# Kernel tuning notes

Measured on AMD Instinct MI355X. Metric: run time of the kernel, lower is better.

## Reference

```python
import jax, jax.numpy as jnp
import numpy as np

L, F, H, T, C, N = 6, 256, 8, 256, 4, 16
HD = F // H
E = 4 * F
D = T * F * C
NS = 2


def setup_inputs() -> dict:
    key = jax.random.key(0)
    ks = iter(jax.random.split(key, 64))
    rn = lambda shape, s=0.02: (jax.random.normal(next(ks), shape, jnp.float32) * s)
    inp = {
        'x': jax.random.normal(next(ks), (N, F, T, C), jnp.float32),
        'Wq': rn((L, HD, HD)), 'Wk': rn((L, HD, HD)), 'Wv': rn((L, HD, HD)),
        'Wo': rn((L, F, F)), 'bo': jnp.zeros((L, F), jnp.float32),
        'ln1_g': jnp.ones((L, F), jnp.float32), 'ln1_b': jnp.zeros((L, F), jnp.float32),
        'ln2_g': jnp.ones((L, F), jnp.float32), 'ln2_b': jnp.zeros((L, F), jnp.float32),
        'ffW1': rn((L, E, F)), 'ffb1': jnp.zeros((L, E), jnp.float32),
        'ffW2': rn((L, F, E)), 'ffb2': jnp.zeros((L, F), jnp.float32),
        'eW1': rn((256, D), 0.005), 'eb1': jnp.zeros((256,), jnp.float32),
        'eg': jnp.ones((256,), jnp.float32), 'ebt': jnp.zeros((256,), jnp.float32),
        'eW2': rn((256, 256)), 'eb2': jnp.zeros((256,), jnp.float32),
        'eW3': rn((256, 256)), 'eb3': jnp.zeros((256,), jnp.float32),
        'eW4': rn((NS, 256)),
        'aW1': rn((256, D), 0.005), 'ab1': jnp.zeros((256,), jnp.float32),
        'ag': jnp.ones((256,), jnp.float32), 'abt': jnp.zeros((256,), jnp.float32),
        'aW2': rn((256, 256)), 'ab2': jnp.zeros((256,), jnp.float32),
        'aW3': rn((256, 256)), 'ab3': jnp.zeros((256,), jnp.float32),
        'aW4': rn((2, 256)),
    }
    return inp


def _layernorm(z, g, b):
    m = z.mean(-1, keepdims=True)
    v = z.var(-1, keepdims=True)
    return (z - m) / jnp.sqrt(v + 1e-5) * g + b


def _forward(x, Wq, Wk, Wv, Wo, bo, ln1_g, ln1_b, ln2_g, ln2_b,
             ffW1, ffb1, ffW2, ffb2,
             eW1, eb1, eg, ebt, eW2, eb2, eW3, eb3, eW4,
             aW1, ab1, ag, abt, aW2, ab2, aW3, ab3, aW4):
    n, f, t, c = x.shape
    # fold cues into batch: (C*N, T, F)
    h = jnp.transpose(x, (3, 0, 2, 1)).reshape(c * n, t, f)
    pos = jnp.linspace(0.0, 1.0, t, dtype=jnp.float32)[None, :, None]  # linspace over time, same per freq
    h = h + pos
    scale = 1.0 / jnp.sqrt(jnp.float32(f))
    for l in range(Wq.shape[0]):
        zr = h.reshape(h.shape[0], t, H, HD)
        q = zr @ Wq[l].T
        k = zr @ Wk[l].T
        v = zr @ Wv[l].T
        att = jax.nn.softmax(jnp.einsum('nqhd,nkhd->nhqk', q, k) * scale, axis=-1)
        o = jnp.einsum('nhqk,nkhd->nqhd', att, v).reshape(h.shape[0], t, f)
        o = o @ Wo[l].T + bo[l]
        x1 = _layernorm(o + h, ln1_g[l], ln1_b[l])
        ff = jax.nn.relu(x1 @ ffW1[l].T + ffb1[l]) @ ffW2[l].T + ffb2[l]
        h = _layernorm(ff + x1, ln2_g[l], ln2_b[l])
    enc = h.reshape(c, n, t, f).transpose(1, 2, 3, 0)  # (N, T, F, C)
    flat = enc.reshape(n, -1)

    def head(W1, b1, g, bt, W2, b2, W3, b3, W4):
        z = flat @ W1.T + b1
        z = z / jnp.sqrt(1.0 + 1e-5) * g + bt  # eval BatchNorm1d, running stats (0, 1)
        z = jax.nn.relu(z)
        z = jax.nn.relu(z @ W2.T + b2)
        z = jax.nn.relu(z @ W3.T + b3)
        return z @ W4.T

    pi = np.float32(np.pi)
    elev = jnp.clip(head(eW1, eb1, eg, ebt, eW2, eb2, eW3, eb3, eW4), -pi / 4, pi / 2)
    azim = jnp.clip(head(aW1, ab1, ag, abt, aW2, ab2, aW3, ab3, aW4), 0.0, 2 * pi)
    cols = []
    for i in range(elev.shape[1]):
        cols.append(elev[:, i])
        cols.append(azim[:, i])
    return jnp.stack(cols, axis=-1)  # (N, 2*Nsound)


def reference(x, Wq, Wk, Wv, Wo, bo, ln1_g, ln1_b, ln2_g, ln2_b,
              ffW1, ffb1, ffW2, ffb2,
              eW1, eb1, eg, ebt, eW2, eb2, eW3, eb3, eW4,
              aW1, ab1, ag, abt, aW2, ab2, aW3, ab3, aW4):
    return _forward(x, Wq, Wk, Wv, Wo, bo, ln1_g, ln1_b, ln2_g, ln2_b,
                    ffW1, ffb1, ffW2, ffb2,
                    eW1, eb1, eg, ebt, eW2, eb2, eW3, eb3, eW4,
                    aW1, ab1, ag, abt, aW2, ab2, aW3, ab3, aW4)
```

## Files before the change

### kernel.cpp

```cpp
#include <hip/hip_runtime.h>
#include <math.h>

#define T_ 256
#define F_ 256
#define B_ 64
#define H_ 8
#define HD_ 32
#define E_ 1024
#define D_ 262144
#define N_ 16
#define M_ 16384

typedef __attribute__((ext_vector_type(8))) short bf16x8;
typedef __attribute__((ext_vector_type(4))) float f32x4;

__global__ __launch_bounds__(256) void build_h(const float* __restrict__ x,
                                               float* __restrict__ h) {
    int idx = blockIdx.x * 256 + threadIdx.x;
    int f = idx & 255;
    int t = (idx >> 8) & 255;
    int b = idx >> 16;
    int c = b >> 4;
    int n = b & 15;
    h[idx] = x[((n * 256 + f) * 256 + t) * 4 + c] + (float)t * (1.0f / 255.0f);
}

__global__ __launch_bounds__(256) void attn_kernel(const float* __restrict__ h,
                                                   const float* __restrict__ Wq,
                                                   const float* __restrict__ Wk,
                                                   const float* __restrict__ Wv,
                                                   float* __restrict__ o) {
    __shared__ float ks[256][32];
    __shared__ float vs[256][32];
    const int b = blockIdx.x >> 3;
    const int hh = blockIdx.x & 7;
    const int t = threadIdx.x;

    const float* zp = h + (b * 256 + t) * 256 + hh * 32;
    float z[32];
#pragma unroll
    for (int e4 = 0; e4 < 8; ++e4) {
        float4 tv = *(const float4*)(zp + e4 * 4);
        z[e4 * 4 + 0] = tv.x; z[e4 * 4 + 1] = tv.y;
        z[e4 * 4 + 2] = tv.z; z[e4 * 4 + 3] = tv.w;
    }

    float q[32];
#pragma unroll
    for (int dg = 0; dg < 8; ++dg) {
        float4 k4, v4;
#pragma unroll
        for (int di = 0; di < 4; ++di) {
            const int d = dg * 4 + di;
            const float* wq = Wq + d * 32;
            const float* wk = Wk + d * 32;
            const float* wv = Wv + d * 32;
            float qd = 0.f, kd = 0.f, vd = 0.f;
#pragma unroll
            for (int e = 0; e < 32; ++e) {
                qd += z[e] * wq[e];
                kd += z[e] * wk[e];
                vd += z[e] * wv[e];
            }
            q[d] = qd * 0.0625f;
            (&k4.x)[di] = kd;
            (&v4.x)[di] = vd;
        }
        *(float4*)&ks[t][dg * 4] = k4;
        *(float4*)&vs[t][dg * 4] = v4;
    }
    __syncthreads();

    float m = -1e30f, lsum = 0.f;
    float oacc[32];
#pragma unroll
    for (int e = 0; e < 32; ++e) oacc[e] = 0.f;

    for (int j = 0; j < 256; ++j) {
        const float4* kp = (const float4*)&ks[j][0];
        float s = 0.f;
#pragma unroll
        for (int e4 = 0; e4 < 8; ++e4) {
            float4 kv = kp[e4];
            s += q[e4 * 4 + 0] * kv.x + q[e4 * 4 + 1] * kv.y +
                 q[e4 * 4 + 2] * kv.z + q[e4 * 4 + 3] * kv.w;
        }
        float mn = fmaxf(m, s);
        float alpha = __expf(m - mn);
        float p = __expf(s - mn);
        lsum = lsum * alpha + p;
        const float4* vp = (const float4*)&vs[j][0];
#pragma unroll
        for (int e4 = 0; e4 < 8; ++e4) {
            float4 vv = vp[e4];
            oacc[e4 * 4 + 0] = oacc[e4 * 4 + 0] * alpha + p * vv.x;
            oacc[e4 * 4 + 1] = oacc[e4 * 4 + 1] * alpha + p * vv.y;
            oacc[e4 * 4 + 2] = oacc[e4 * 4 + 2] * alpha + p * vv.z;
            oacc[e4 * 4 + 3] = oacc[e4 * 4 + 3] * alpha + p * vv.w;
        }
        m = mn;
    }
    const float inv = 1.0f / lsum;
    float* op = o + (b * 256 + t) * 256 + hh * 32;
#pragma unroll
    for (int e4 = 0; e4 < 8; ++e4) {
        float4 ov;
        ov.x = oacc[e4 * 4 + 0] * inv; ov.y = oacc[e4 * 4 + 1] * inv;
        ov.z = oacc[e4 * 4 + 2] * inv; ov.w = oacc[e4 * 4 + 3] * inv;
        *(float4*)(op + e4 * 4) = ov;
    }
}

#define LDST 40

struct GemmLds {
    short Ahi[128][LDST];
    short Alo[128][LDST];
    short Whi[128][LDST];
    short Wlo[128][LDST];
};

__device__ inline void split2(float a0, float a1, unsigned& hi, unsigned& lo) {
    unsigned u0 = __float_as_uint(a0), u1 = __float_as_uint(a1);
    hi = __builtin_amdgcn_perm(u1, u0, 0x07060302);
    float r0 = a0 - __uint_as_float(u0 & 0xffff0000u);
    float r1 = a1 - __uint_as_float(u1 & 0xffff0000u);
    lo = __builtin_amdgcn_perm(__float_as_uint(r1), __float_as_uint(r0), 0x07060302);
}

__global__ __launch_bounds__(256, 2) void gemm_mfma(const float* __restrict__ A,
                                                    const float* __restrict__ W,
                                                    const float* __restrict__ bias,
                                                    float* __restrict__ C,
                                                    int M, int Nn, int K, int doRelu) {
    __shared__ GemmLds lds;
    const int tid = threadIdx.x;
    const int row0 = blockIdx.y * 128, col0 = blockIdx.x * 128;
    const int wave = tid >> 6, lane = tid & 63;
    const int wr = wave >> 1, wc = wave & 1;
    const int lrow = tid >> 3;
    const int lcol = (tid & 7) * 4;

    f32x4 acc[4][4];
#pragma unroll
    for (int i = 0; i < 4; ++i)
#pragma unroll
        for (int j = 0; j < 4; ++j) acc[i][j] = (f32x4){0.f, 0.f, 0.f, 0.f};

    float4 abuf[4], wbuf[4];
#pragma unroll
    for (int jj = 0; jj < 4; ++jj) {
        abuf[jj] = *(const float4*)&A[(size_t)(row0 + jj * 32 + lrow) * K + lcol];
        wbuf[jj] = *(const float4*)&W[(size_t)(col0 + jj * 32 + lrow) * K + lcol];
    }

    for (int k0 = 0; k0 < K; k0 += 32) {
#pragma unroll
        for (int jj = 0; jj < 4; ++jj) {
            const int row = jj * 32 + lrow;
            unsigned h01, l01, h23, l23;
            split2(abuf[jj].x, abuf[jj].y, h01, l01);
            split2(abuf[jj].z, abuf[jj].w, h23, l23);
            *(uint2*)&lds.Ahi[row][lcol] = make_uint2(h01, h23);
            *(uint2*)&lds.Alo[row][lcol] = make_uint2(l01, l23);
            split2(wbuf[jj].x, wbuf[jj].y, h01, l01);
            split2(wbuf[jj].z, wbuf[jj].w, h23, l23);
            *(uint2*)&lds.Whi[row][lcol] = make_uint2(h01, h23);
            *(uint2*)&lds.Wlo[row][lcol] = make_uint2(l01, l23);
        }
        __syncthreads();

        if (k0 + 32 < K) {
#pragma unroll
            for (int jj = 0; jj < 4; ++jj) {
                abuf[jj] = *(const float4*)&A[(size_t)(row0 + jj * 32 + lrow) * K + k0 + 32 + lcol];
                wbuf[jj] = *(const float4*)&W[(size_t)(col0 + jj * 32 + lrow) * K + k0 + 32 + lcol];
            }
        }

        const int fr = lane & 15, koff = (lane >> 4) * 8;
        bf16x8 ahi[4], alo[4], whi[4], wlo[4];
#pragma unroll
        for (int i = 0; i < 4; ++i) {
            ahi[i] = *(const bf16x8*)&lds.Ahi[wr * 64 + i * 16 + fr][koff];
            alo[i] = *(const bf16x8*)&lds.Alo[wr * 64 + i * 16 + fr][koff];
        }
#pragma unroll
        for (int j = 0; j < 4; ++j) {
            whi[j] = *(const bf16x8*)&lds.Whi[wc * 64 + j * 16 + fr][koff];
            wlo[j] = *(const bf16x8*)&lds.Wlo[wc * 64 + j * 16 + fr][koff];
        }
#pragma unroll
        for (int i = 0; i < 4; ++i)
#pragma unroll
            for (int j = 0; j < 4; ++j) {
                acc[i][j] = __builtin_amdgcn_mfma_f32_16x16x32_bf16(alo[i], whi[j], acc[i][j], 0, 0, 0);
                acc[i][j] = __builtin_amdgcn_mfma_f32_16x16x32_bf16(ahi[i], wlo[j], acc[i][j], 0, 0, 0);
                acc[i][j] = __builtin_amdgcn_mfma_f32_16x16x32_bf16(ahi[i], whi[j], acc[i][j], 0, 0, 0);
            }
        __syncthreads();
    }

    const int fr = lane & 15, rg = (lane >> 4) * 4;
#pragma unroll
    for (int j = 0; j < 4; ++j) {
        const int col = col0 + wc * 64 + j * 16 + fr;
        const float bv = bias[col];
#pragma unroll
        for (int i = 0; i < 4; ++i) {
#pragma unroll
            for (int r = 0; r < 4; ++r) {
                const int row = row0 + wr * 64 + i * 16 + rg + r;
                float v = acc[i][j][r] + bv;
                if (doRelu) v = fmaxf(v, 0.f);
                C[(size_t)row * Nn + col] = v;
            }
        }
    }
}

__global__ __launch_bounds__(256) void ln_residual(const float* __restrict__ A,
                                                   const float* __restrict__ R,
                                                   const float* __restrict__ g,
                                                   const float* __restrict__ b,
                                                   float* __restrict__ O) {
    const int row = blockIdx.x;
    const int tid = threadIdx.x;
    float v = A[row * 256 + tid] + R[row * 256 + tid];
    float s = v, sq = v * v;
#pragma unroll
    for (int off = 32; off > 0; off >>= 1) {
        s += __shfl_down(s, off, 64);
        sq += __shfl_down(sq, off, 64);
    }
    __shared__ float ss[4], ssq[4];
    const int wave = tid >> 6, lane = tid & 63;
    if (lane == 0) { ss[wave] = s; ssq[wave] = sq; }
    __syncthreads();
    float S = ss[0] + ss[1] + ss[2] + ss[3];
    float SQ = ssq[0] + ssq[1] + ssq[2] + ssq[3];
    float mean = S * (1.0f / 256.0f);
    float var = SQ * (1.0f / 256.0f) - mean * mean;
    float inv = rsqrtf(var + 1e-5f);
    O[row * 256 + tid] = (v - mean) * inv * g[tid] + b[tid];
}

__global__ __launch_bounds__(256) void head_gemm(const float* __restrict__ h,
                                                 const float* __restrict__ eW1,
                                                 const float* __restrict__ aW1,
                                                 float* __restrict__ zraw) {
    const int bx = blockIdx.x;
    const int jt = bx >> 4;
    const int chunk = bx & 15;
    const int jj0 = jt * 4;
    const int head = jj0 >> 8;
    const int jl0 = jj0 & 255;
    const float* W = (head ? aW1 : eW1) + (size_t)jl0 * D_;
    const int tid = threadIdx.x;

    float acc[4][16];
#pragma unroll
    for (int jb = 0; jb < 4; ++jb)
#pragma unroll
        for (int n = 0; n < 16; ++n) acc[jb][n] = 0.f;

    for (int s = 0; s < 16; ++s) {
        const int d4 = chunk * 16384 + s * 1024 + tid * 4;
        const int tf = d4 >> 2;
        float4 wv[4];
#pragma unroll
        for (int jb = 0; jb < 4; ++jb)
            wv[jb] = *(const float4*)(W + (size_t)jb * D_ + d4);
#pragma unroll
        for (int c = 0; c < 4; ++c) {
            const float* hp = h + c * 1048576 + tf;
            float fl[16];
#pragma unroll
            for (int n = 0; n < 16; ++n) fl[n] = hp[n * 65536];
#pragma unroll
            for (int jb = 0; jb < 4; ++jb) {
                const float w = (&wv[jb].x)[c];
#pragma unroll
                for (int n = 0; n < 16; ++n) acc[jb][n] += w * fl[n];
            }
        }
    }

    const int lane = tid & 63;
#pragma unroll
    for (int jb = 0; jb < 4; ++jb) {
#pragma unroll
        for (int n = 0; n < 16; ++n) {
            float v = acc[jb][n];
            v += __shfl_down(v, 32, 64);
            v += __shfl_down(v, 16, 64);
            v += __shfl_down(v, 8, 64);
            v += __shfl_down(v, 4, 64);
            v += __shfl_down(v, 2, 64);
            v += __shfl_down(v, 1, 64);
            if (lane == 0)
                atomicAdd(&zraw[head * 4096 + n * 256 + jl0 + jb], v);
        }
    }
}

__global__ __launch_bounds__(256) void zero_kernel(float* __restrict__ p) {
    p[blockIdx.x * 256 + threadIdx.x] = 0.f;
}

__global__ __launch_bounds__(256) void mlp_head(const float* __restrict__ zr,
                                                const float* __restrict__ b1,
                                                const float* __restrict__ g,
                                                const float* __restrict__ bt,
                                                const float* __restrict__ W2,
                                                const float* __restrict__ b2,
                                                const float* __restrict__ W3,
                                                const float* __restrict__ b3,
                                                const float* __restrict__ W4,
                                                float* __restrict__ out,
                                                float lo, float hi, int coff) {
    __shared__ float za[256], zb[256];
    const int n = blockIdx.x, j = threadIdx.x;
    float z = zr[n * 256 + j] + b1[j];
    z = z * 0.99999500003749969f * g[j] + bt[j];
    za[j] = fmaxf(z, 0.f);
    __syncthreads();
    float a = b2[j];
    for (int e = 0; e < 256; ++e) a += za[e] * W2[j * 256 + e];
    zb[j] = fmaxf(a, 0.f);
    __syncthreads();
    a = b3[j];
    for (int e = 0; e < 256; ++e) a += zb[e] * W3[j * 256 + e];
    za[j] = fmaxf(a, 0.f);
    __syncthreads();
    if (j < 2) {
        float v = 0.f;
        for (int e = 0; e < 256; ++e) v += za[e] * W4[j * 256 + e];
        v = fminf(fmaxf(v, lo), hi);
        out[n * 4 + 2 * j + coff] = v;
    }
}

extern "C" void kernel_launch(void* const* d_in, const int* in_sizes, int n_in,
                              void* d_out, int out_size, void* d_ws, size_t ws_size,
                              hipStream_t stream) {
    const float* x     = (const float*)d_in[0];
    const float* Wq    = (const float*)d_in[1];
    const float* Wk    = (const float*)d_in[2];
    const float* Wv    = (const float*)d_in[3];
    const float* Wo    = (const float*)d_in[4];
    const float* bo    = (const float*)d_in[5];
    const float* ln1g  = (const float*)d_in[6];
    const float* ln1b  = (const float*)d_in[7];
    const float* ln2g  = (const float*)d_in[8];
    const float* ln2b  = (const float*)d_in[9];
    const float* ffW1  = (const float*)d_in[10];
    const float* ffb1  = (const float*)d_in[11];
    const float* ffW2  = (const float*)d_in[12];
    const float* ffb2  = (const float*)d_in[13];
    const float* eW1   = (const float*)d_in[14];
    const float* eb1   = (const float*)d_in[15];
    const float* eg    = (const float*)d_in[16];
    const float* ebt   = (const float*)d_in[17];
    const float* eW2   = (const float*)d_in[18];
    const float* eb2   = (const float*)d_in[19];
    const float* eW3   = (const float*)d_in[20];
    const float* eb3   = (const float*)d_in[21];
    const float* eW4   = (const float*)d_in[22];
    const float* aW1   = (const float*)d_in[23];
    const float* ab1   = (const float*)d_in[24];
    const float* ag    = (const float*)d_in[25];
    const float* abt   = (const float*)d_in[26];
    const float* aW2   = (const float*)d_in[27];
    const float* ab2   = (const float*)d_in[28];
    const float* aW3   = (const float*)d_in[29];
    const float* ab3   = (const float*)d_in[30];
    const float* aW4   = (const float*)d_in[31];
    float* out = (float*)d_out;

    float* ws   = (float*)d_ws;
    float* h    = ws;
    float* ao   = ws + 4194304;
    float* tmp  = ws + 8388608;
    float* x1   = ws + 12582912;
    float* ff1  = ws + 16777216;
    float* zraw = ws + 33554432;

    build_h<<<16384, 256, 0, stream>>>(x, h);

    for (int l = 0; l < 6; ++l) {
        attn_kernel<<<512, 256, 0, stream>>>(h, Wq + l * 1024, Wk + l * 1024,
                                             Wv + l * 1024, ao);
        gemm_mfma<<<dim3(2, 128), 256, 0, stream>>>(ao, Wo + l * 65536, bo + l * 256,
                                                    tmp, M_, 256, 256, 0);
        ln_residual<<<16384, 256, 0, stream>>>(tmp, h, ln1g + l * 256, ln1b + l * 256, x1);
        gemm_mfma<<<dim3(8, 128), 256, 0, stream>>>(x1, ffW1 + l * 262144, ffb1 + l * 1024,
                                                    ff1, M_, 1024, 256, 1);
        gemm_mfma<<<dim3(2, 128), 256, 0, stream>>>(ff1, ffW2 + l * 262144, ffb2 + l * 256,
                                                    tmp, M_, 256, 1024, 0);
        ln_residual<<<16384, 256, 0, stream>>>(tmp, x1, ln2g + l * 256, ln2b + l * 256, h);
    }

    zero_kernel<<<32, 256, 0, stream>>>(zraw);
    head_gemm<<<2048, 256, 0, stream>>>(h, eW1, aW1, zraw);

    const float pi = 3.14159265358979323846f;
    mlp_head<<<16, 256, 0, stream>>>(zraw, eb1, eg, ebt, eW2, eb2, eW3, eb3, eW4,
                                     out, -pi / 4.f, pi / 2.f, 0);
    mlp_head<<<16, 256, 0, stream>>>(zraw + 4096, ab1, ag, abt, aW2, ab2, aW3, ab3, aW4,
                                     out, 0.f, 2.f * pi, 1);
}
```

Measured before the change: 2.555 ms.

## Restructure head GEMM to stage activations in shared memory and split by K-chunk

The big head GEMM (512x262144 weights against 16 batch rows) is reorganised. Each block now stages a 256-element slice of the encoder output for all 64 (cue, batch) columns in LDS and reuses it across all 256 output rows of one head. Previously every block re-read strided activations from global memory. Each thread handles 4 output rows for one cue, and results are reduced with xor shuffles across 4 lanes before atomics into zraw. The change also shrinks the grid from 2048 to 512 blocks, with more work per block and more atomics per block.

```diff
diff --git a/kernel.cpp b/kernel.cpp
--- a/kernel.cpp
+++ b/kernel.cpp
@@ -249,58 +249,72 @@
                                                  const float* __restrict__ eW1,
                                                  const float* __restrict__ aW1,
                                                  float* __restrict__ zraw) {
-    const int bx = blockIdx.x;
-    const int jt = bx >> 4;
-    const int chunk = bx & 15;
-    const int jj0 = jt * 4;
-    const int head = jj0 >> 8;
-    const int jl0 = jj0 & 255;
-    const float* W = (head ? aW1 : eW1) + (size_t)jl0 * D_;
+    __shared__ float hs[256][64];
     const int tid = threadIdx.x;
-
-    float acc[4][16];
-#pragma unroll
-    for (int jb = 0; jb < 4; ++jb)
-#pragma unroll
-        for (int n = 0; n < 16; ++n) acc[jb][n] = 0.f;
-
-    for (int s = 0; s < 16; ++s) {
-        const int d4 = chunk * 16384 + s * 1024 + tid * 4;
-        const int tf = d4 >> 2;
-        float4 wv[4];
-#pragma unroll
-        for (int jb = 0; jb < 4; ++jb)
-            wv[jb] = *(const float4*)(W + (size_t)jb * D_ + d4);
-#pragma unroll
-        for (int c = 0; c < 4; ++c) {
-            const float* hp = h + c * 1048576 + tf;
-            float fl[16];
-#pragma unroll
-            for (int n = 0; n < 16; ++n) fl[n] = hp[n * 65536];
-#pragma unroll
-            for (int jb = 0; jb < 4; ++jb) {
-                const float w = (&wv[jb].x)[c];
-#pragma unroll
-                for (int n = 0; n < 16; ++n) acc[jb][n] += w * fl[n];
+    const int jt = blockIdx.x >> 8;
+    const int kc = blockIdx.x & 255;
+    const int tf0 = kc * 256;
+
+    {
+        const int w = tid >> 6;
+        const int cn = tid & 63;
+        const int c = cn >> 4, n = cn & 15;
+        const float* hp = h + c * 1048576 + n * 65536 + tf0 + w * 64;
+#pragma unroll
+        for (int k4 = 0; k4 < 16; ++k4) {
+            float4 hv = *(const float4*)(hp + k4 * 4);
+            hs[w * 64 + k4 * 4 + 0][cn] = hv.x;
+            hs[w * 64 + k4 * 4 + 1][cn] = hv.y;
+            hs[w * 64 + k4 * 4 + 2][cn] = hv.z;
+            hs[w * 64 + k4 * 4 + 3][cn] = hv.w;
+        }
+    }
+    __syncthreads();
+
+    const int jg = tid >> 2;
+    const int c = tid & 3;
+    const float* Wp = (jt ? aW1 : eW1) + (size_t)(jg * 4) * D_ + kc * 1024 + c;
+
+    f32x4 acc[4][4];
+#pragma unroll
+    for (int jj = 0; jj < 4; ++jj)
+#pragma unroll
+        for (int n4 = 0; n4 < 4; ++n4) acc[jj][n4] = (f32x4){0.f, 0.f, 0.f, 0.f};
+
+#pragma unroll 4
+    for (int i = 0; i < 256; ++i) {
+        const float w0 = Wp[i * 4];
+        const float w1 = Wp[i * 4 + D_];
+        const float w2 = Wp[i * 4 + 2 * D_];
+        const float w3 = Wp[i * 4 + 3 * D_];
+        const f32x4* hv = (const f32x4*)&hs[i][c * 16];
+        const f32x4 h0 = hv[0], h1 = hv[1], h2 = hv[2], h3 = hv[3];
+        acc[0][0] += w0 * h0; acc[0][1] += w0 * h1; acc[0][2] += w0 * h2; acc[0][3] += w0 * h3;
+        acc[1][0] += w1 * h0; acc[1][1] += w1 * h1; acc[1][2] += w1 * h2; acc[1][3] += w1 * h3;
+        acc[2][0] += w2 * h0; acc[2][1] += w2 * h1; acc[2][2] += w2 * h2; acc[2][3] += w2 * h3;
+        acc[3][0] += w3 * h0; acc[3][1] += w3 * h1; acc[3][2] += w3 * h2; acc[3][3] += w3 * h3;
+    }
+
+#pragma unroll
+    for (int jj = 0; jj < 4; ++jj)
+#pragma unroll
+        for (int n4 = 0; n4 < 4; ++n4)
+#pragma unroll
+            for (int q = 0; q < 4; ++q) {
+                float v = acc[jj][n4][q];
+                v += __shfl_xor(v, 1, 64);
+                v += __shfl_xor(v, 2, 64);
+                acc[jj][n4][q] = v;
             }
-        }
-    }
-
-    const int lane = tid & 63;
-#pragma unroll
-    for (int jb = 0; jb < 4; ++jb) {
-#pragma unroll
-        for (int n = 0; n < 16; ++n) {
-            float v = acc[jb][n];
-            v += __shfl_down(v, 32, 64);
-            v += __shfl_down(v, 16, 64);
-            v += __shfl_down(v, 8, 64);
-            v += __shfl_down(v, 4, 64);
-            v += __shfl_down(v, 2, 64);
-            v += __shfl_down(v, 1, 64);
-            if (lane == 0)
-                atomicAdd(&zraw[head * 4096 + n * 256 + jl0 + jb], v);
-        }
+    if (c == 0) {
+        float* zp = zraw + jt * 4096 + jg * 4;
+#pragma unroll
+        for (int jj = 0; jj < 4; ++jj)
+#pragma unroll
+            for (int n4 = 0; n4 < 4; ++n4)
+#pragma unroll
+                for (int q = 0; q < 4; ++q)
+                    atomicAdd(&zp[(n4 * 4 + q) * 256 + jj], acc[jj][n4][q]);
     }
 }
 
@@ -402,7 +416,7 @@
     }
 
     zero_kernel<<<32, 256, 0, stream>>>(zraw);
-    head_gemm<<<2048, 256, 0, stream>>>(h, eW1, aW1, zraw);
+    head_gemm<<<512, 256, 0, stream>>>(h, eW1, aW1, zraw);
 
     const float pi = 3.14159265358979323846f;
     mlp_head<<<16, 256, 0, stream>>>(zraw, eb1, eg, ebt, eW2, eb2, eW3, eb3, eW4,
```

Result: no change. 2.580 ms (+1.0%).

## Run head GEMM on bf16 MFMA with hi/lo split-precision emulation

Applied to the files above, without the earlier changes.

Replaces the scalar FP32 FMA head GEMM (16 samples × 512 outputs × 262144 reduction) with an MFMA kernel. The activations are pre-split into bf16 hi/lo planes in a new pass, and the weights are split on the fly, using three bf16 MFMAs per tile to approximate FP32 precision. Each block stages a 512-wide K slice of B in swizzled LDS, reduces across waves in LDS, and atomically accumulates the result. This adds an extra kernel plus its global traffic, and accuracy now depends on the 3-term bf16 split. split2 is assumed to be defined in the hidden part of the file.

```diff
diff --git a/kernel.cpp b/kernel.cpp
--- a/kernel.cpp
+++ b/kernel.cpp
@@ -13,6 +13,7 @@
 
 typedef __attribute__((ext_vector_type(8))) short bf16x8;
 typedef __attribute__((ext_vector_type(4))) float f32x4;
+typedef unsigned short u16;
 
 __global__ __launch_bounds__(256) void build_h(const float* __restrict__ x,
                                                float* __restrict__ h) {
@@ -245,61 +246,123 @@
     O[row * 256 + tid] = (v - mean) * inv * g[tid] + b[tid];
 }
 
-__global__ __launch_bounds__(256) void head_gemm(const float* __restrict__ h,
-                                                 const float* __restrict__ eW1,
-                                                 const float* __restrict__ aW1,
-                                                 float* __restrict__ zraw) {
-    const int bx = blockIdx.x;
-    const int jt = bx >> 4;
-    const int chunk = bx & 15;
-    const int jj0 = jt * 4;
-    const int head = jj0 >> 8;
-    const int jl0 = jj0 & 255;
-    const float* W = (head ? aW1 : eW1) + (size_t)jl0 * D_;
+__global__ __launch_bounds__(256) void bsplit_kernel(const float* __restrict__ h,
+                                                     u16* __restrict__ Bhi,
+                                                     u16* __restrict__ Blo) {
+    const int idx = blockIdx.x * 256 + threadIdx.x;
+    const int n = idx >> 16;
+    const int tf = idx & 65535;
+    const float f0 = h[n * 65536 + tf];
+    const float f1 = h[1048576 + n * 65536 + tf];
+    const float f2 = h[2097152 + n * 65536 + tf];
+    const float f3 = h[3145728 + n * 65536 + tf];
+    unsigned h01, l01, h23, l23;
+    split2(f0, f1, h01, l01);
+    split2(f2, f3, h23, l23);
+    *(uint2*)&Bhi[(size_t)n * D_ + tf * 4] = make_uint2(h01, h23);
+    *(uint2*)&Blo[(size_t)n * D_ + tf * 4] = make_uint2(l01, l23);
+}
+
+struct HeadLds {
+    union {
+        struct { u16 bhi[16][512]; u16 blo[16][512]; } b;
+        float red[2][4096];
+    };
+};
+
+__global__ __launch_bounds__(256, 4) void head_gemm(const float* __restrict__ eW1,
+                                                    const float* __restrict__ aW1,
+                                                    const u16* __restrict__ Bhi,
+                                                    const u16* __restrict__ Blo,
+                                                    float* __restrict__ zraw) {
+    __shared__ HeadLds lds;
     const int tid = threadIdx.x;
-
-    float acc[4][16];
-#pragma unroll
-    for (int jb = 0; jb < 4; ++jb)
-#pragma unroll
-        for (int n = 0; n < 16; ++n) acc[jb][n] = 0.f;
-
-    for (int s = 0; s < 16; ++s) {
-        const int d4 = chunk * 16384 + s * 1024 + tid * 4;
-        const int tf = d4 >> 2;
-        float4 wv[4];
-#pragma unroll
-        for (int jb = 0; jb < 4; ++jb)
-            wv[jb] = *(const float4*)(W + (size_t)jb * D_ + d4);
-#pragma unroll
-        for (int c = 0; c < 4; ++c) {
-            const float* hp = h + c * 1048576 + tf;
-            float fl[16];
-#pragma unroll
-            for (int n = 0; n < 16; ++n) fl[n] = hp[n * 65536];
-#pragma unroll
-            for (int jb = 0; jb < 4; ++jb) {
-                const float w = (&wv[jb].x)[c];
-#pragma unroll
-                for (int n = 0; n < 16; ++n) acc[jb][n] += w * fl[n];
-            }
-        }
-    }
-
-    const int lane = tid & 63;
-#pragma unroll
-    for (int jb = 0; jb < 4; ++jb) {
-#pragma unroll
-        for (int n = 0; n < 16; ++n) {
-            float v = acc[jb][n];
-            v += __shfl_down(v, 32, 64);
-            v += __shfl_down(v, 16, 64);
-            v += __shfl_down(v, 8, 64);
-            v += __shfl_down(v, 4, 64);
-            v += __shfl_down(v, 2, 64);
-            v += __shfl_down(v, 1, 64);
-            if (lane == 0)
-                atomicAdd(&zraw[head * 4096 + n * 256 + jl0 + jb], v);
+    const int head = blockIdx.x & 1;
+    const int kb = blockIdx.x >> 1;
+    const int K0 = kb * 512;
+    const int wv = tid >> 6, lane = tid & 63;
+    const int fr = lane & 15;
+    const int kg = lane >> 4;
+
+    {
+        const int u = lane;
+        for (int rr = 0; rr < 4; ++rr) {
+            const int n = rr * 4 + wv;
+            const int us = u ^ (n & 7);
+            *(uint4*)&lds.b.bhi[n][us * 8] = *(const uint4*)&Bhi[(size_t)n * D_ + K0 + u * 8];
+            *(uint4*)&lds.b.blo[n][us * 8] = *(const uint4*)&Blo[(size_t)n * D_ + K0 + u * 8];
+        }
+    }
+    __syncthreads();
+
+    f32x4 acc[16];
+#pragma unroll
+    for (int jt = 0; jt < 16; ++jt) acc[jt] = (f32x4){0.f, 0.f, 0.f, 0.f};
+
+    const int kq = wv * 128;
+    const float* ap0 = (head ? aW1 : eW1) + (size_t)fr * D_ + K0 + kq + kg * 8;
+
+#define HG_ADDR(it) (ap0 + (size_t)((it) >> 2) * (16 * D_) + ((it) & 3) * 32)
+    float4 c0 = *(const float4*)HG_ADDR(0);
+    float4 c1 = *(const float4*)(HG_ADDR(0) + 4);
+    float4 m0 = *(const float4*)HG_ADDR(1);
+    float4 m1 = *(const float4*)(HG_ADDR(1) + 4);
+#pragma unroll
+    for (int it = 0; it < 64; ++it) {
+        float4 n0, n1;
+        if (it < 62) {
+            n0 = *(const float4*)HG_ADDR(it + 2);
+            n1 = *(const float4*)(HG_ADDR(it + 2) + 4);
+        }
+        const int u = (kq + (it & 3) * 32 + kg * 8) >> 3;
+        const int us = u ^ (fr & 7);
+        bf16x8 bh = *(const bf16x8*)&lds.b.bhi[fr][us * 8];
+        bf16x8 bl = *(const bf16x8*)&lds.b.blo[fr][us * 8];
+        unsigned h01, l01, h23, l23, h45, l45, h67, l67;
+        split2(c0.x, c0.y, h01, l01);
+        split2(c0.z, c0.w, h23, l23);
+        split2(c1.x, c1.y, h45, l45);
+        split2(c1.z, c1.w, h67, l67);
+        union { bf16x8 v; unsigned u[4]; } ah, al;
+        ah.u[0] = h01; ah.u[1] = h23; ah.u[2] = h45; ah.u[3] = h67;
+        al.u[0] = l01; al.u[1] = l23; al.u[2] = l45; al.u[3] = l67;
+        const int jt = it >> 2;
+        acc[jt] = __builtin_amdgcn_mfma_f32_16x16x32_bf16(al.v, bh, acc[jt], 0, 0, 0);
+        acc[jt] = __builtin_amdgcn_mfma_f32_16x16x32_bf16(ah.v, bl, acc[jt], 0, 0, 0);
+        acc[jt] = __builtin_amdgcn_mfma_f32_16x16x32_bf16(ah.v, bh, acc[jt], 0, 0, 0);
+        c0 = m0; c1 = m1; m0 = n0; m1 = n1;
+    }
+#undef HG_ADDR
+
+    const int ru = (fr * 4 + kg) * 4;
+    __syncthreads();
+    if (wv >= 2) {
+#pragma unroll
+        for (int jt = 0; jt < 16; ++jt)
+            *(f32x4*)&lds.red[wv - 2][jt * 256 + ru] = acc[jt];
+    }
+    __syncthreads();
+    if (wv < 2) {
+#pragma unroll
+        for (int jt = 0; jt < 16; ++jt)
+            acc[jt] += *(const f32x4*)&lds.red[wv][jt * 256 + ru];
+    }
+    __syncthreads();
+    if (wv == 1) {
+#pragma unroll
+        for (int jt = 0; jt < 16; ++jt)
+            *(f32x4*)&lds.red[0][jt * 256 + ru] = acc[jt];
+    }
+    __syncthreads();
+    if (wv == 0) {
+#pragma unroll
+        for (int jt = 0; jt < 16; ++jt) {
+            f32x4 v = acc[jt] + *(const f32x4*)&lds.red[0][jt * 256 + ru];
+            float* zp = zraw + head * 4096 + fr * 256 + jt * 16 + kg * 4;
+            atomicAdd(&zp[0], v[0]);
+            atomicAdd(&zp[1], v[1]);
+            atomicAdd(&zp[2], v[2]);
+            atomicAdd(&zp[3], v[3]);
         }
     }
 }
@@ -401,8 +464,11 @@
         ln_residual<<<16384, 256, 0, stream>>>(tmp, x1, ln2g + l * 256, ln2b + l * 256, h);
     }
 
+    u16* Bhi = (u16*)(ws + 16777216);
+    u16* Blo = (u16*)(ws + 16777216 + 2097152);
+    bsplit_kernel<<<4096, 256, 0, stream>>>(h, Bhi, Blo);
     zero_kernel<<<32, 256, 0, stream>>>(zraw);
-    head_gemm<<<2048, 256, 0, stream>>>(h, eW1, aW1, zraw);
+    head_gemm<<<1024, 256, 0, stream>>>(eW1, aW1, Bhi, Blo, zraw);
 
     const float pi = 3.14159265358979323846f;
     mlp_head<<<16, 256, 0, stream>>>(zraw, eb1, eg, ebt, eW2, eb2, eW3, eb3, eW4,
```

Measured after the change: 2.493 ms. 2.4% less time.
